# Kernel optimization log

Measured on AMD Instinct MI355X. Metric: run time of the kernel, lower is better.

The kernel has to match this reference:

```python
import jax, jax.numpy as jnp
import numpy as np

NUM_HEAD = 8
B, NO, LQ, LC, D = 16, 512, 512, 512, 1024


def setup_inputs() -> dict:
    key = jax.random.key(0)
    ks = jax.random.split(key, 32)
    s = 0.02

    def lin(i, din, dout):
        w = jax.random.normal(ks[i], (din, dout), jnp.float32) * s
        b = jax.random.normal(ks[i + 1], (dout,), jnp.float32) * s
        return w, b

    v = jax.random.normal(ks[20], (B, NO, D), jnp.float32)
    q = jax.random.normal(ks[21], (B, LQ, D), jnp.float32)
    c = jax.random.normal(ks[22], (B, LC, D), jnp.float32)
    # binary float masks; force first position valid so mask.sum > 0
    v_mask = jax.random.randint(ks[23], (B, NO), 0, 2).astype(jnp.float32).at[:, 0].set(1.0)
    q_mask = jax.random.randint(ks[24], (B, LQ), 0, 2).astype(jnp.float32).at[:, 0].set(1.0)
    c_mask = jax.random.randint(ks[25], (B, LC), 0, 2).astype(jnp.float32).at[:, 0].set(1.0)
    v4q_w, v4q_b = lin(0, D, D)
    q4v_w, q4v_b = lin(2, D, D)
    v_lin_w, v_lin_b = lin(4, D, 3 * D)
    q_lin_w, q_lin_b = lin(6, D, 3 * D)
    c_lin_w, c_lin_b = lin(8, D, 3 * D)
    v_out_w, v_out_b = lin(10, D, D)
    q_out_w, q_out_b = lin(12, D, D)
    c_out_w, c_out_b = lin(14, D, D)
    m_v_k = jax.random.normal(ks[16], (1, 1, D), jnp.float32) * s
    m_v_v = jax.random.normal(ks[17], (1, 1, D), jnp.float32) * s
    m_c_k = jax.random.normal(ks[18], (1, 1, D), jnp.float32) * s
    m_c_v = jax.random.normal(ks[19], (1, 1, D), jnp.float32) * s
    return dict(v=v, q=q, c=c, v_mask=v_mask, q_mask=q_mask, c_mask=c_mask,
                v4q_w=v4q_w, v4q_b=v4q_b, q4v_w=q4v_w, q4v_b=q4v_b,
                v_lin_w=v_lin_w, v_lin_b=v_lin_b, q_lin_w=q_lin_w, q_lin_b=q_lin_b,
                c_lin_w=c_lin_w, c_lin_b=c_lin_b,
                m_v_k=m_v_k, m_v_v=m_v_v, m_c_k=m_c_k, m_c_v=m_c_v,
                v_out_w=v_out_w, v_out_b=v_out_b, q_out_w=q_out_w, q_out_b=q_out_b,
                c_out_w=c_out_w, c_out_b=c_out_b)


def _attn(q_in, k_in, v_in, kmask):
    # q_in [B,Sq,D], k_in/v_in [B,Sk,D], kmask [B,Sk]. Vectorized over heads
    # (replaces the per-head Python loop + cat in the torch source).
    Bs, Sq, Dm = q_in.shape
    Sk = k_in.shape[1]
    dh = Dm // NUM_HEAD
    qh = q_in.reshape(Bs, Sq, NUM_HEAD, dh)
    kh = k_in.reshape(Bs, Sk, NUM_HEAD, dh)
    vh = v_in.reshape(Bs, Sk, NUM_HEAD, dh)
    scores = jnp.einsum('bqhd,bkhd->bhqk', qh, kh)
    # torch: masked_fill(-1e9) then divide by sqrt(d_head) -> replicate exactly
    scores = jnp.where(kmask[:, None, None, :] == 0, jnp.float32(-1e9), scores) / (dh ** 0.5)
    w = jax.nn.softmax(scores, axis=-1)
    out = jnp.einsum('bhqk,bkhd->bqhd', w, vh)
    return out.reshape(Bs, Sq, Dm)


def _forward(v, q, c, v_mask, q_mask, c_mask,
             v4q_w, v4q_b, q4v_w, q4v_b,
             v_lin_w, v_lin_b, q_lin_w, q_lin_b, c_lin_w, c_lin_b,
             m_v_k, m_v_v, m_c_k, m_c_v,
             v_out_w, v_out_b, q_out_w, q_out_b, c_out_w, c_out_b):
    Bs = v.shape[0]
    Dm = v_out_w.shape[0]
    relu, sig = jax.nn.relu, jax.nn.sigmoid
    v_mean = (v * v_mask[:, :, None]).sum(1) / v_mask.sum(1, keepdims=True)
    q_mean = (q * q_mask[:, :, None]).sum(1) / q_mask.sum(1, keepdims=True)
    v4q_gate = sig(relu(v_mean) @ v4q_w + v4q_b)[:, None, :]  # gates q's q/k
    q4v_gate = sig(relu(q_mean) @ q4v_w + q4v_b)[:, None, :]  # gates v's q/k
    v_trans = (relu(v) @ v_lin_w + v_lin_b) * v_mask[:, :, None]
    q_trans = (relu(q) @ q_lin_w + q_lin_b) * q_mask[:, :, None]
    c_trans = (relu(c) @ c_lin_w + c_lin_b) * c_mask[:, :, None]
    v_k, v_q, v_v = jnp.split(v_trans, 3, axis=2)
    q_k, q_q, q_v = jnp.split(q_trans, 3, axis=2)
    c_k, c_q, c_v = jnp.split(c_trans, 3, axis=2)
    # memory tokens: k scaled by sqrt(D), v scaled by sqrt(mv)=1 (as in torch)
    mvk = (Dm ** 0.5) * jnp.broadcast_to(m_v_k, (Bs, 1, Dm))
    mvv = jnp.broadcast_to(m_v_v, (Bs, 1, Dm))
    v_k = jnp.concatenate([mvk, v_k], axis=1)
    v_v = jnp.concatenate([mvv, v_v], axis=1)
    v_kmask = jnp.concatenate([jnp.ones((Bs, 1), v_mask.dtype), v_mask], axis=1)
    mck = (Dm ** 0.5) * jnp.broadcast_to(m_c_k, (Bs, 1, Dm))
    mcv = jnp.broadcast_to(m_c_v, (Bs, 1, Dm))
    c_k = jnp.concatenate([mck, c_k], axis=1)
    c_v = jnp.concatenate([mcv, c_v], axis=1)
    c_kmask = jnp.concatenate([jnp.ones((Bs, 1), c_mask.dtype), c_mask], axis=1)
    new_vq = (1.0 + q4v_gate) * v_q
    new_vk = (1.0 + q4v_gate) * v_k
    new_qq = (1.0 + v4q_gate) * q_q
    new_qk = (1.0 + v4q_gate) * q_k
    v_update = _attn(new_vq, new_vk, v_v, v_kmask)
    q_update = _attn(new_qq, new_qk, q_v, q_mask)
    c_update = _attn(c_q, c_k, c_v, c_kmask)
    updated_v = (v + v_update) @ v_out_w + v_out_b
    updated_q = (q + q_update) @ q_out_w + q_out_b
    updated_c = (c + c_update) @ c_out_w + c_out_b
    return updated_v, updated_q, updated_c


def reference(v, q, c, v_mask, q_mask, c_mask,
              v4q_w, v4q_b, q4v_w, q4v_b,
              v_lin_w, v_lin_b, q_lin_w, q_lin_b, c_lin_w, c_lin_b,
              m_v_k, m_v_v, m_c_k, m_c_v,
              v_out_w, v_out_b, q_out_w, q_out_b, c_out_w, c_out_b):
    return _forward(v, q, c, v_mask, q_mask, c_mask,
                    v4q_w, v4q_b, q4v_w, q4v_b,
                    v_lin_w, v_lin_b, q_lin_w, q_lin_b, c_lin_w, c_lin_b,
                    m_v_k, m_v_v, m_c_k, m_c_v,
                    v_out_w, v_out_b, q_out_w, q_out_b, c_out_w, c_out_b)
```

## Files before the change

kernel.cpp:

```cpp
#include <hip/hip_runtime.h>
#include <stdint.h>

typedef __attribute__((ext_vector_type(8))) short s16x8;
typedef __attribute__((ext_vector_type(4))) float f32x4;

#define DM 1024
#define TOK 512
#define LDK 3072

static __device__ __forceinline__ float bf2f(short u) {
  union { unsigned int i; float f; } x;
  x.i = ((unsigned int)(unsigned short)u) << 16;
  return x.f;
}
static __device__ __forceinline__ short f2bf(float f) {
  union { float f; unsigned int i; } x; x.f = f;
  unsigned int r = x.i + 0x7FFFu + ((x.i >> 16) & 1u);
  return (short)(r >> 16);
}
static __device__ __forceinline__ f32x4 fzero4() {
  f32x4 z; z[0]=0.f; z[1]=0.f; z[2]=0.f; z[3]=0.f; return z;
}
static __device__ __forceinline__ s16x8 szero8() {
  s16x8 z; z[0]=0; z[1]=0; z[2]=0; z[3]=0; z[4]=0; z[5]=0; z[6]=0; z[7]=0; return z;
}
static __device__ __forceinline__ void gl_lds16(const short* g, short* s) {
  __builtin_amdgcn_global_load_lds((const __attribute__((address_space(1))) void*)g,
                                   (__attribute__((address_space(3))) void*)s, 16, 0, 0);
}

#define MFMA(a, b, c) __builtin_amdgcn_mfma_f32_16x16x32_bf16(a, b, c, 0, 0, 0)

struct CastArgs { const float* x[3]; short* xb[3]; const float* mask[3]; };
__global__ __launch_bounds__(256) void cast_relu_kernel(CastArgs a) {
  const float* x = a.x[blockIdx.y];
  short* xb = a.xb[blockIdx.y];
  const float* mk = a.mask[blockIdx.y];
  int row = blockIdx.x * 2 + (threadIdx.x >> 7);
  if (mk[row] == 0.f) return;
  size_t i = (size_t)row * DM + (threadIdx.x & 127) * 8;
  float4 v0 = *(const float4*)(x + i);
  float4 v1 = *(const float4*)(x + i + 4);
  s16x8 o;
  o[0] = f2bf(fmaxf(v0.x, 0.f)); o[1] = f2bf(fmaxf(v0.y, 0.f));
  o[2] = f2bf(fmaxf(v0.z, 0.f)); o[3] = f2bf(fmaxf(v0.w, 0.f));
  o[4] = f2bf(fmaxf(v1.x, 0.f)); o[5] = f2bf(fmaxf(v1.y, 0.f));
  o[6] = f2bf(fmaxf(v1.z, 0.f)); o[7] = f2bf(fmaxf(v1.w, 0.f));
  *(s16x8*)(xb + i) = o;
}

__global__ __launch_bounds__(1024) void mean_kernel(const float* __restrict__ v,
                                                    const float* __restrict__ q,
                                                    const float* __restrict__ vmask,
                                                    const float* __restrict__ qmask,
                                                    float* __restrict__ vmean,
                                                    float* __restrict__ qmean) {
  __shared__ float part[4][256];
  __shared__ float msh[4];
  int dl = threadIdx.x & 255;
  int rg = threadIdx.x >> 8;
  int d = blockIdx.x * 256 + dl;
  int b = blockIdx.y;
  const float* x; const float* mk; float* out;
  if (blockIdx.z == 0) { x = v; mk = vmask; out = vmean; }
  else                 { x = q; mk = qmask; out = qmean; }
  const float* xp = x + ((size_t)b * TOK) * DM + d;
  const float* mp = mk + b * TOK;
  float s = 0.f, ms = 0.f;
  int r0 = rg * 128;
#pragma unroll 4
  for (int r = 0; r < 128; ++r) {
    float m = mp[r0 + r];
    ms += m;
    s += xp[(size_t)(r0 + r) * DM] * m;
  }
  part[rg][dl] = s;
  if (dl == 0) msh[rg] = ms;
  __syncthreads();
  if (rg == 0) {
    float st = part[0][dl] + part[1][dl] + part[2][dl] + part[3][dl];
    float mst = msh[0] + msh[1] + msh[2] + msh[3];
    out[b * DM + d] = st / mst;
  }
}

struct TransArgs { const float* w[3]; short* wt[3]; };
__global__ void transpose_cast_kernel(TransArgs a, int K, int N) {
  __shared__ float tile[32][33];
  const float* w = a.w[blockIdx.z];
  short* wt = a.wt[blockIdx.z];
  int n0 = blockIdx.x * 32, k0 = blockIdx.y * 32;
  int tx = threadIdx.x, ty = threadIdx.y;
#pragma unroll
  for (int i = 0; i < 32; i += 8)
    tile[ty + i][tx] = w[(size_t)(k0 + ty + i) * N + n0 + tx];
  __syncthreads();
#pragma unroll
  for (int i = 0; i < 32; i += 8)
    wt[(size_t)(n0 + ty + i) * K + k0 + tx] = f2bf(tile[tx][ty + i]);
}

__global__ __launch_bounds__(1024) void gate_kernel(const float* __restrict__ vmean,
                                                    const float* __restrict__ qmean,
                                                    const float* __restrict__ v4q_w,
                                                    const float* __restrict__ v4q_b,
                                                    const float* __restrict__ q4v_w,
                                                    const float* __restrict__ q4v_b,
                                                    float* __restrict__ gate_q,
                                                    float* __restrict__ gate_v) {
  __shared__ float part[4][256];
  int nl = threadIdx.x & 255;
  int kg = threadIdx.x >> 8;
  int n = blockIdx.x * 256 + nl;
  int b = blockIdx.y;
  const float* mean; const float* w; const float* bias; float* out;
  if (blockIdx.z == 0) { mean = vmean; w = v4q_w; bias = v4q_b; out = gate_q; }
  else                 { mean = qmean; w = q4v_w; bias = q4v_b; out = gate_v; }
  const float* mp = mean + b * DM;
  float acc = 0.f;
  int k0 = kg * 256;
#pragma unroll 4
  for (int k = 0; k < 256; ++k) {
    float mv = mp[k0 + k];
    mv = mv > 0.f ? mv : 0.f;
    acc += mv * w[(size_t)(k0 + k) * DM + n];
  }
  part[kg][nl] = acc;
  __syncthreads();
  if (kg == 0) {
    float a = part[0][nl] + part[1][nl] + part[2][nl] + part[3][nl] + bias[n];
    out[b * DM + n] = 1.f + 1.f / (1.f + __expf(-a));
  }
}

__global__ void kmem_kernel(const float* __restrict__ m_v_k, const float* __restrict__ m_c_k,
                            const float* __restrict__ gate_v,
                            float* __restrict__ kmem_v, float* __restrict__ kmem_c) {
  int d = threadIdx.x;
  int b = blockIdx.x;
  if (b < 16) kmem_v[b * DM + d] = 32.0f * m_v_k[d] * gate_v[b * DM + d];
  else        kmem_c[d] = 32.0f * m_c_k[d];
}

struct CompArgs { const float* mask[3]; int* idx; int* nv; };
__global__ __launch_bounds__(64) void compact_kernel(CompArgs a) {
  int b = blockIdx.x, mod = blockIdx.y;
  const float* mk = a.mask[mod] + b * TOK;
  int* idx = a.idx + (mod * 16 + b) * TOK;
  int l = threadIdx.x;
  int base = 0;
#pragma unroll 1
  for (int ch = 0; ch < 8; ++ch) {
    int pos = ch * 64 + l;
    bool valid = mk[pos] != 0.f;
    unsigned long long bal = __ballot(valid);
    int pre = __popcll(bal & ((1ull << l) - 1ull));
    if (valid) idx[base + pre] = pos;
    base += __popcll(bal);
  }
  if (l == 0) a.nv[mod * 16 + b] = base;
}

struct GemmArgs {
  const short* A[3]; const short* BT[3];
  const float* bias[3]; const float* gate[3];
  short* outB[3]; float* outF[3];
  const int* idx;
  const int* nv;
};
__global__ __launch_bounds__(512) void gemm_kernel(GemmArgs ga, int N, int K) {
  __shared__ short As[128 * 64];
  __shared__ short Bs[128 * 64];
  int z = blockIdx.z;
  const short* A = ga.A[z];
  const short* BT = ga.BT[z];
  const float* bias = ga.bias[z];
  const float* gate = ga.gate[z];
  short* outB = ga.outB[z];
  float* outF = ga.outF[z];

  int bx = blockIdx.x;
  int b = bx >> 2, m0c = (bx & 3) * 128;
  int nvb = TOK;
  const int* idxb = nullptr;
  if (ga.nv != nullptr) {
    nvb = ga.nv[z * 16 + b];
    if (m0c >= nvb) return;
    idxb = ga.idx + (z * 16 + b) * TOK;
  }
  int n0 = blockIdx.y * 128;
  int tid = threadIdx.x;
  int w = tid >> 6, l = tid & 63;
  int wr = w >> 2, wc = w & 3;
  int lg = l >> 4, lo = l & 15;

  int cc = (l & 7) ^ (l >> 3);
  const short* pa[2];
  const short* pb[2];
#pragma unroll
  for (int i = 0; i < 2; ++i) {
    int row = (w * 2 + i) * 8 + (l >> 3);
    int rg = m0c + row;
    if (idxb != nullptr) rg = idxb[(m0c + row < nvb) ? (m0c + row) : 0];
    pa[i] = A + ((size_t)b * TOK + rg) * K + cc * 8;
    pb[i] = BT + (size_t)(n0 + row) * K + cc * 8;
  }

  f32x4 acc[4][2];
#pragma unroll
  for (int i = 0; i < 4; ++i)
#pragma unroll
    for (int j = 0; j < 2; ++j) acc[i][j] = fzero4();

  for (int k0 = 0; k0 < K; k0 += 64) {
#pragma unroll
    for (int i = 0; i < 2; ++i) {
      gl_lds16(pa[i] + k0, As + (w * 2 + i) * 512);
      gl_lds16(pb[i] + k0, Bs + (w * 2 + i) * 512);
    }
    __syncthreads();
#pragma unroll
    for (int ks = 0; ks < 2; ++ks) {
      int lc = ks * 4 + lg;
      s16x8 af[4], bfr[2];
#pragma unroll
      for (int i = 0; i < 4; ++i) {
        int ar = wr * 64 + i * 16 + lo;
        af[i] = *(const s16x8*)(As + ar * 64 + ((lc ^ (ar & 7)) * 8));
      }
#pragma unroll
      for (int j = 0; j < 2; ++j) {
        int br = wc * 32 + j * 16 + lo;
        bfr[j] = *(const s16x8*)(Bs + br * 64 + ((lc ^ (br & 7)) * 8));
      }
#pragma unroll
      for (int i = 0; i < 4; ++i)
#pragma unroll
        for (int j = 0; j < 2; ++j)
          acc[i][j] = MFMA(af[i], bfr[j], acc[i][j]);
    }
    __syncthreads();
  }

#pragma unroll
  for (int i = 0; i < 4; ++i)
#pragma unroll
    for (int j = 0; j < 2; ++j) {
      int rowc = m0c + wr * 64 + i * 16 + (lg << 2);
      int col = n0 + wc * 32 + j * 16 + lo;
      float cs = 1.f;
      if (gate != nullptr && col < 2048) cs = gate[b * DM + (col & 1023)];
      float bv = bias[col];
#pragma unroll
      for (int r = 0; r < 4; ++r) {
        if (rowc + r >= nvb) continue;
        float val = (acc[i][j][r] + bv) * cs;
        size_t orow = (size_t)b * TOK + rowc + r;
        if (outB != nullptr) outB[orow * N + col] = f2bf(val);
        else                 outF[orow * N + col] = val;
      }
    }
}

struct AttnArgs {
  const short* kqv[3];
  const float* kmem[3];
  const float* vmem[3];
  const float* xin[3];
  short* xu[3];
  const int* idx;
  const int* nv;
  int kmem_bstride[3];
};

__global__ __launch_bounds__(512) void attn_kernel(AttnArgs args) {
  __shared__ short Ks[64 * 128];
  __shared__ short Vs[8 * 1032];
  __shared__ short Ps[8 * 1216];
  int bid = blockIdx.x;
  int mod = bid >> 9;
  int r9 = bid & 511;
  int x = r9 & 7, jj = r9 >> 3;
  int p = x * 16 + (jj & 15), qt = jj >> 4;
  int b = p >> 3, h = p & 7;

  int nvb = args.nv[mod * 16 + b];
  if (qt * 128 >= nvb) return;

  const short* kqv  = args.kqv[mod];
  const float* kmem = args.kmem[mod];
  const float* vmem = args.vmem[mod];
  const float* xin  = args.xin[mod];
  short* xu = args.xu[mod];
  const int* idxb = args.idx + (mod * 16 + b) * TOK;
  int kmem_bs = args.kmem_bstride[mod];

  int tid = threadIdx.x;
  int w = tid >> 6, l = tid & 63;
  int lg = l >> 4, lo = l & 15;
  size_t rowbase = (size_t)b * TOK;
  int q0 = qt * 128 + w * 16;
  const float scale = 0.08838834764831845f;
  short* Pw = Ps + w * 1216;
  int nkt = (nvb + 63) >> 6;

  s16x8 ones;
#pragma unroll
  for (int j = 0; j < 8; ++j) ones[j] = (short)0x3F80;

  int qrow = q0 + lo;
  s16x8 qf[4];
#pragma unroll
  for (int c = 0; c < 4; ++c)
    qf[c] = (qrow < nvb)
      ? *(const s16x8*)(kqv + (rowbase + qrow) * LDK + 1024 + h * 128 + c * 32 + lg * 8)
      : szero8();

  float m;
  f32x4 oacc[9];
#pragma unroll
  for (int c = 0; c < 9; ++c) oacc[c] = fzero4();

  if (kmem != nullptr) {
    const float* km = kmem + (size_t)b * kmem_bs + h * 128;
    float part = 0.f;
#pragma unroll
    for (int c = 0; c < 4; ++c)
#pragma unroll
      for (int j = 0; j < 8; ++j)
        part += bf2f(qf[c][j]) * km[c * 32 + lg * 8 + j];
    part += __shfl_xor(part, 16);
    part += __shfl_xor(part, 32);
    float sm = part * scale;
    float sm4[4], w4[4];
#pragma unroll
    for (int r = 0; r < 4; ++r) sm4[r] = __shfl(sm, lg * 4 + r);
    m = fmaxf(fmaxf(sm4[0], sm4[1]), fmaxf(sm4[2], sm4[3]));
#pragma unroll
    for (int r = 0; r < 4; ++r) w4[r] = __expf(sm4[r] - m);
#pragma unroll
    for (int c = 0; c < 8; ++c) {
      float vv = vmem[h * 128 + c * 16 + lo];
#pragma unroll
      for (int r = 0; r < 4; ++r) oacc[c][r] = w4[r] * vv;
    }
#pragma unroll
    for (int r = 0; r < 4; ++r) oacc[8][r] = w4[r];
  } else {
    m = -3.0e38f;
  }

  int c8A = 2 * w, c8B = 2 * w + 1;
  s16x8 vregA = (l < nvb)
    ? *(const s16x8*)(kqv + (rowbase + l) * LDK + 2048 + h * 128 + c8A * 8) : szero8();
  s16x8 vregB = (l < nvb)
    ? *(const s16x8*)(kqv + (rowbase + l) * LDK + 2048 + h * 128 + c8B * 8) : szero8();

#pragma unroll 1
  for (int kt = 0; kt < nkt; ++kt) {
    __syncthreads();
#pragma unroll
    for (int i = 0; i < 2; ++i) {
      int inst = w * 2 + i;
      int row = inst * 4 + lg;
      int csrc = (l & 15) ^ (row & 7);
      gl_lds16(kqv + (rowbase + kt * 64 + row) * LDK + h * 128 + csrc * 8,
               Ks + inst * 512);
    }
    {
      short* baseA = Vs + (l >> 3) * 1032 + c8A * 64 + (l & 7);
      short* baseB = Vs + (l >> 3) * 1032 + c8B * 64 + (l & 7);
#pragma unroll
      for (int j = 0; j < 8; ++j) baseA[j * 8] = vregA[j];
#pragma unroll
      for (int j = 0; j < 8; ++j) baseB[j * 8] = vregB[j];
    }
    __syncthreads();

    if (kt + 1 < nkt) {
      int row2 = (kt + 1) * 64 + l;
      vregA = (row2 < nvb)
        ? *(const s16x8*)(kqv + (rowbase + row2) * LDK + 2048 + h * 128 + c8A * 8) : szero8();
      vregB = (row2 < nvb)
        ? *(const s16x8*)(kqv + (rowbase + row2) * LDK + 2048 + h * 128 + c8B * 8) : szero8();
    }

    f32x4 s4[4];
#pragma unroll
    for (int sub = 0; sub < 4; ++sub) {
      f32x4 acc = fzero4();
      int krow = sub * 16 + lo;
#pragma unroll
      for (int cc = 0; cc < 4; ++cc) {
        s16x8 kf = *(const s16x8*)(Ks + krow * 128 + (((cc * 4 + lg) ^ (lo & 7)) * 8));
        acc = MFMA(qf[cc], kf, acc);
      }
      s4[sub] = acc;
    }

    int pos0 = kt * 64 + lo;
    float a[4][4];
    float pmax = -3.0e38f;
#pragma unroll
    for (int r = 0; r < 4; ++r) {
      a[0][r] = (pos0      < nvb) ? s4[0][r] * scale : -1e9f;
      a[1][r] = (pos0 + 16 < nvb) ? s4[1][r] * scale : -1e9f;
      a[2][r] = (pos0 + 32 < nvb) ? s4[2][r] * scale : -1e9f;
      a[3][r] = (pos0 + 48 < nvb) ? s4[3][r] * scale : -1e9f;
      pmax = fmaxf(pmax, fmaxf(fmaxf(a[0][r], a[1][r]), fmaxf(a[2][r], a[3][r])));
    }
    pmax = fmaxf(pmax, __shfl_xor(pmax, 1));
    pmax = fmaxf(pmax, __shfl_xor(pmax, 2));
    pmax = fmaxf(pmax, __shfl_xor(pmax, 4));
    pmax = fmaxf(pmax, __shfl_xor(pmax, 8));
    if (!__all(pmax - m <= 8.0f)) {
      float nm = fmaxf(m, pmax);
      float f = __expf(m - nm);
#pragma unroll
      for (int c = 0; c < 9; ++c)
#pragma unroll
        for (int r = 0; r < 4; ++r) oacc[c][r] *= f;
      m = nm;
    }

#pragma unroll
    for (int sub = 0; sub < 4; ++sub)
#pragma unroll
      for (int r = 0; r < 4; ++r)
        Pw[(lg * 4 + r) * 76 + sub * 16 + lo] = f2bf(__expf(a[sub][r] - m));

    s16x8 pf0 = *(const s16x8*)(Pw + lo * 76 + lg * 8);
    s16x8 pf1 = *(const s16x8*)(Pw + lo * 76 + 32 + lg * 8);
#pragma unroll
    for (int c = 0; c < 8; ++c) {
      s16x8 vf0 = *(const s16x8*)(Vs + lg * 1032 + (c * 16 + lo) * 8);
      s16x8 vf1 = *(const s16x8*)(Vs + (4 + lg) * 1032 + (c * 16 + lo) * 8);
      oacc[c] = MFMA(pf0, vf0, oacc[c]);
      oacc[c] = MFMA(pf1, vf1, oacc[c]);
    }
    oacc[8] = MFMA(pf0, ones, oacc[8]);
    oacc[8] = MFMA(pf1, ones, oacc[8]);
  }

  int orig[4];
#pragma unroll
  for (int r = 0; r < 4; ++r) {
    int crow = q0 + lg * 4 + r;
    orig[r] = (crow < nvb) ? idxb[crow] : -1;
  }
  float invl[4];
#pragma unroll
  for (int r = 0; r < 4; ++r) invl[r] = 1.f / oacc[8][r];
#pragma unroll
  for (int c = 0; c < 8; ++c)
#pragma unroll
    for (int r = 0; r < 4; ++r) {
      if (orig[r] < 0) continue;
      size_t row = rowbase + orig[r];
      int col = h * 128 + c * 16 + lo;
      float val = oacc[c][r] * invl[r] + xin[row * DM + col];
      xu[row * DM + col] = f2bf(val);
    }
}

struct UniArgs {
  const short* kqv[3]; const float* mask[3]; const float* mem[3];
  const float* xin[3]; short* xu[3]; const int* nv;
};
__global__ __launch_bounds__(1024) void uniform_fill_kernel(UniArgs a) {
  __shared__ float part[8][1024];
  int b = blockIdx.x, mod = blockIdx.y;
  int nvb = a.nv[mod * 16 + b];
  const short* kv = a.kqv[mod];
  int tid = threadIdx.x;
  int g = tid >> 7;
  int dd = tid & 127;

  f32x4 p0 = fzero4(), p1 = fzero4();
#pragma unroll 2
  for (int r = g; r < nvb; r += 8) {
    s16x8 vv = *(const s16x8*)(kv + ((size_t)b * TOK + r) * LDK + 2048 + dd * 8);
#pragma unroll
    for (int j = 0; j < 4; ++j) { p0[j] += bf2f(vv[j]); p1[j] += bf2f(vv[4 + j]); }
  }
  *(f32x4*)&part[g][dd * 8] = p0;
  *(f32x4*)&part[g][dd * 8 + 4] = p1;
  __syncthreads();
  {
    float s = 0.f;
#pragma unroll
    for (int gg = 0; gg < 8; ++gg) s += part[gg][tid];
    float denom = (float)nvb;
    if (a.mem[mod] != nullptr) { s += a.mem[mod][tid]; denom += 1.f; }
    __syncthreads();
    part[0][tid] = s / denom;
  }
  __syncthreads();
  float avg[8];
#pragma unroll
  for (int j = 0; j < 8; ++j) avg[j] = part[0][dd * 8 + j];

  const float* mk = a.mask[mod] + b * TOK;
  const float* x = a.xin[mod];
  short* xu = a.xu[mod];
#pragma unroll 1
  for (int rb = 0; rb < TOK; rb += 8) {
    int r = rb + g;
    if (mk[r] != 0.f) continue;
    size_t base = ((size_t)b * TOK + r) * DM + dd * 8;
    float4 x0 = *(const float4*)(x + base);
    float4 x1 = *(const float4*)(x + base + 4);
    s16x8 o;
    o[0] = f2bf(x0.x + avg[0]); o[1] = f2bf(x0.y + avg[1]);
    o[2] = f2bf(x0.z + avg[2]); o[3] = f2bf(x0.w + avg[3]);
    o[4] = f2bf(x1.x + avg[4]); o[5] = f2bf(x1.y + avg[5]);
    o[6] = f2bf(x1.z + avg[6]); o[7] = f2bf(x1.w + avg[7]);
    *(s16x8*)(xu + base) = o;
  }
}

extern "C" void kernel_launch(void* const* d_in, const int* in_sizes, int n_in,
                              void* d_out, int out_size, void* d_ws, size_t ws_size,
                              hipStream_t stream) {
  const float* v      = (const float*)d_in[0];
  const float* q      = (const float*)d_in[1];
  const float* c      = (const float*)d_in[2];
  const float* v_mask = (const float*)d_in[3];
  const float* q_mask = (const float*)d_in[4];
  const float* c_mask = (const float*)d_in[5];
  const float* v4q_w  = (const float*)d_in[6];
  const float* v4q_b  = (const float*)d_in[7];
  const float* q4v_w  = (const float*)d_in[8];
  const float* q4v_b  = (const float*)d_in[9];
  const float* v_lin_w = (const float*)d_in[10];
  const float* v_lin_b = (const float*)d_in[11];
  const float* q_lin_w = (const float*)d_in[12];
  const float* q_lin_b = (const float*)d_in[13];
  const float* c_lin_w = (const float*)d_in[14];
  const float* c_lin_b = (const float*)d_in[15];
  const float* m_v_k  = (const float*)d_in[16];
  const float* m_v_v  = (const float*)d_in[17];
  const float* m_c_k  = (const float*)d_in[18];
  const float* m_c_v  = (const float*)d_in[19];
  const float* v_out_w = (const float*)d_in[20];
  const float* v_out_b = (const float*)d_in[21];
  const float* q_out_w = (const float*)d_in[22];
  const float* q_out_b = (const float*)d_in[23];
  const float* c_out_w = (const float*)d_in[24];
  const float* c_out_b = (const float*)d_in[25];

  const size_t MB = 1024ull * 1024ull;
  char* ws = (char*)d_ws;
  short* xbf_v = (short*)(ws + 0 * MB);
  short* xbf_q = (short*)(ws + 16 * MB);
  short* xbf_c = (short*)(ws + 32 * MB);
  short* wt_lin_v = (short*)(ws + 48 * MB);
  short* wt_lin_q = (short*)(ws + 54 * MB);
  short* wt_lin_c = (short*)(ws + 60 * MB);
  short* wt_out_v = (short*)(ws + 66 * MB);
  short* wt_out_q = (short*)(ws + 68 * MB);
  short* wt_out_c = (short*)(ws + 70 * MB);
  short* kqv_v = (short*)(ws + 72 * MB);
  short* kqv_q = (short*)(ws + 120 * MB);
  short* kqv_c = (short*)(ws + 168 * MB);
  float* vmean  = (float*)(ws + 216 * MB);
  float* qmean  = vmean + 16 * 1024;
  float* gate_q = qmean + 16 * 1024;
  float* gate_v = gate_q + 16 * 1024;
  float* kmem_v = gate_v + 16 * 1024;
  float* kmem_c = kmem_v + 16 * 1024;
  int* idxbuf = (int*)(ws + 217 * MB);
  int* nvbuf  = (int*)(ws + 218 * MB);

  CompArgs cpa;
  cpa.mask[0] = v_mask; cpa.mask[1] = q_mask; cpa.mask[2] = c_mask;
  cpa.idx = idxbuf; cpa.nv = nvbuf;
  compact_kernel<<<dim3(16, 3), 64, 0, stream>>>(cpa);

  CastArgs ca;
  ca.x[0] = v; ca.x[1] = q; ca.x[2] = c;
  ca.xb[0] = xbf_v; ca.xb[1] = xbf_q; ca.xb[2] = xbf_c;
  ca.mask[0] = v_mask; ca.mask[1] = q_mask; ca.mask[2] = c_mask;
  cast_relu_kernel<<<dim3(4096, 3), 256, 0, stream>>>(ca);
  mean_kernel<<<dim3(4, 16, 2), 1024, 0, stream>>>(v, q, v_mask, q_mask, vmean, qmean);

  TransArgs tl;
  tl.w[0] = v_lin_w; tl.w[1] = q_lin_w; tl.w[2] = c_lin_w;
  tl.wt[0] = wt_lin_v; tl.wt[1] = wt_lin_q; tl.wt[2] = wt_lin_c;
  transpose_cast_kernel<<<dim3(96, 32, 3), dim3(32, 8), 0, stream>>>(tl, 1024, 3072);
  TransArgs to;
  to.w[0] = v_out_w; to.w[1] = q_out_w; to.w[2] = c_out_w;
  to.wt[0] = wt_out_v; to.wt[1] = wt_out_q; to.wt[2] = wt_out_c;
  transpose_cast_kernel<<<dim3(32, 32, 3), dim3(32, 8), 0, stream>>>(to, 1024, 1024);

  gate_kernel<<<dim3(4, 16, 2), 1024, 0, stream>>>(vmean, qmean, v4q_w, v4q_b, q4v_w, q4v_b,
                                                   gate_q, gate_v);
  kmem_kernel<<<17, 1024, 0, stream>>>(m_v_k, m_c_k, gate_v, kmem_v, kmem_c);

  GemmArgs gt;
  gt.A[0] = xbf_v; gt.A[1] = xbf_q; gt.A[2] = xbf_c;
  gt.BT[0] = wt_lin_v; gt.BT[1] = wt_lin_q; gt.BT[2] = wt_lin_c;
  gt.bias[0] = v_lin_b; gt.bias[1] = q_lin_b; gt.bias[2] = c_lin_b;
  gt.gate[0] = gate_v; gt.gate[1] = gate_q; gt.gate[2] = nullptr;
  gt.outB[0] = kqv_v; gt.outB[1] = kqv_q; gt.outB[2] = kqv_c;
  gt.outF[0] = nullptr; gt.outF[1] = nullptr; gt.outF[2] = nullptr;
  gt.idx = idxbuf; gt.nv = nvbuf;
  gemm_kernel<<<dim3(64, 24, 3), 512, 0, stream>>>(gt, 3072, 1024);

  AttnArgs aa;
  aa.kqv[0] = kqv_v; aa.kqv[1] = kqv_q; aa.kqv[2] = kqv_c;
  aa.kmem[0] = kmem_v; aa.kmem[1] = nullptr; aa.kmem[2] = kmem_c;
  aa.vmem[0] = m_v_v; aa.vmem[1] = nullptr; aa.vmem[2] = m_c_v;
  aa.xin[0] = v; aa.xin[1] = q; aa.xin[2] = c;
  aa.xu[0] = xbf_v; aa.xu[1] = xbf_q; aa.xu[2] = xbf_c;
  aa.idx = idxbuf; aa.nv = nvbuf;
  aa.kmem_bstride[0] = 1024; aa.kmem_bstride[1] = 0; aa.kmem_bstride[2] = 0;
  attn_kernel<<<1536, 512, 0, stream>>>(aa);

  UniArgs ua;
  ua.kqv[0] = kqv_v; ua.kqv[1] = kqv_q; ua.kqv[2] = kqv_c;
  ua.mask[0] = v_mask; ua.mask[1] = q_mask; ua.mask[2] = c_mask;
  ua.mem[0] = m_v_v; ua.mem[1] = nullptr; ua.mem[2] = m_c_v;
  ua.xin[0] = v; ua.xin[1] = q; ua.xin[2] = c;
  ua.xu[0] = xbf_v; ua.xu[1] = xbf_q; ua.xu[2] = xbf_c;
  ua.nv = nvbuf;
  uniform_fill_kernel<<<dim3(16, 3), 1024, 0, stream>>>(ua);

  float* outp = (float*)d_out;
  GemmArgs go;
  go.A[0] = xbf_v; go.A[1] = xbf_q; go.A[2] = xbf_c;
  go.BT[0] = wt_out_v; go.BT[1] = wt_out_q; go.BT[2] = wt_out_c;
  go.bias[0] = v_out_b; go.bias[1] = q_out_b; go.bias[2] = c_out_b;
  go.gate[0] = nullptr; go.gate[1] = nullptr; go.gate[2] = nullptr;
  go.outB[0] = nullptr; go.outB[1] = nullptr; go.outB[2] = nullptr;
  go.outF[0] = outp; go.outF[1] = outp + 8388608; go.outF[2] = outp + 16777216;
  go.idx = nullptr; go.nv = nullptr;
  gemm_kernel<<<dim3(64, 8, 3), 512, 0, stream>>>(go, 1024, 1024);
}
```

Baseline: 508.6 us.

## Double-buffer LDS tiles in GEMM to overlap global loads with MFMA

Allocates two LDS buffers for the A and B tiles and prefetches the next K-slice with direct global-to-LDS loads while the current slice feeds the MFMAs. Explicit vmcnt/lgkmcnt waits and raw s_barrier calls replace the __syncthreads pairs. The goal is to hide global memory latency behind compute. In exchange, LDS use per block doubles to 64 KB, which can lower occupancy, and the hand-counted vmcnt has to match the number of outstanding loads exactly.

```diff
diff --git a/kernel.cpp b/kernel.cpp
--- a/kernel.cpp
+++ b/kernel.cpp
@@ -169,8 +169,8 @@
   const int* nv;
 };
 __global__ __launch_bounds__(512) void gemm_kernel(GemmArgs ga, int N, int K) {
-  __shared__ short As[128 * 64];
-  __shared__ short Bs[128 * 64];
+  __shared__ short As[2][128 * 64];
+  __shared__ short Bs[2][128 * 64];
   int z = blockIdx.z;
   const short* A = ga.A[z];
   const short* BT = ga.BT[z];
@@ -212,13 +212,29 @@
 #pragma unroll
     for (int j = 0; j < 2; ++j) acc[i][j] = fzero4();
 
-  for (int k0 = 0; k0 < K; k0 += 64) {
-#pragma unroll
-    for (int i = 0; i < 2; ++i) {
-      gl_lds16(pa[i] + k0, As + (w * 2 + i) * 512);
-      gl_lds16(pb[i] + k0, Bs + (w * 2 + i) * 512);
-    }
-    __syncthreads();
+#pragma unroll
+  for (int i = 0; i < 2; ++i) {
+    gl_lds16(pa[i], &As[0][(w * 2 + i) * 512]);
+    gl_lds16(pb[i], &Bs[0][(w * 2 + i) * 512]);
+  }
+
+  int nIter = K >> 6;
+  int cur = 0;
+  for (int t = 0; t < nIter; ++t) {
+    if (t + 1 < nIter) {
+      int nk = (t + 1) << 6;
+#pragma unroll
+      for (int i = 0; i < 2; ++i) {
+        gl_lds16(pa[i] + nk, &As[cur ^ 1][(w * 2 + i) * 512]);
+        gl_lds16(pb[i] + nk, &Bs[cur ^ 1][(w * 2 + i) * 512]);
+      }
+      asm volatile("s_waitcnt vmcnt(4)" ::: "memory");
+    } else {
+      asm volatile("s_waitcnt vmcnt(0)" ::: "memory");
+    }
+    __builtin_amdgcn_s_barrier();
+    __builtin_amdgcn_sched_barrier(0);
+
 #pragma unroll
     for (int ks = 0; ks < 2; ++ks) {
       int lc = ks * 4 + lg;
@@ -226,12 +242,12 @@
 #pragma unroll
       for (int i = 0; i < 4; ++i) {
         int ar = wr * 64 + i * 16 + lo;
-        af[i] = *(const s16x8*)(As + ar * 64 + ((lc ^ (ar & 7)) * 8));
+        af[i] = *(const s16x8*)(&As[cur][0] + ar * 64 + ((lc ^ (ar & 7)) * 8));
       }
 #pragma unroll
       for (int j = 0; j < 2; ++j) {
         int br = wc * 32 + j * 16 + lo;
-        bfr[j] = *(const s16x8*)(Bs + br * 64 + ((lc ^ (br & 7)) * 8));
+        bfr[j] = *(const s16x8*)(&Bs[cur][0] + br * 64 + ((lc ^ (br & 7)) * 8));
       }
 #pragma unroll
       for (int i = 0; i < 4; ++i)
@@ -239,7 +255,10 @@
         for (int j = 0; j < 2; ++j)
           acc[i][j] = MFMA(af[i], bfr[j], acc[i][j]);
     }
-    __syncthreads();
+    asm volatile("s_waitcnt lgkmcnt(0)" ::: "memory");
+    __builtin_amdgcn_s_barrier();
+    __builtin_amdgcn_sched_barrier(0);
+    cur ^= 1;
   }
 
 #pragma unroll
```

Result: slower. 542.8 us (+6.7%).
